# Optimization experiments

Measured on AMD Instinct MI355X. Metric: run time of the kernel, lower is better.

## Reference

```python
import jax, jax.numpy as jnp
import numpy as np
from jax import lax

K_ITERS = 35

def _conv3x3_same(x, w, b):
    # x: [B,1,H,W], w: [1,1,3,3]
    y = lax.conv_general_dilated(x, w, window_strides=(1, 1),
                                 padding=((1, 1), (1, 1)),
                                 dimension_numbers=('NCHW', 'OIHW', 'NCHW'))
    return y + b.reshape(1, -1, 1, 1)

def _maxpool3x3_same(v):
    # 3x3 max pool, stride 1, padding 1 (torch MaxPool2d(kernel=3, stride=1, padding=1))
    return lax.reduce_window(v, -jnp.inf, lax.max,
                             window_dimensions=(1, 1, 3, 3),
                             window_strides=(1, 1, 1, 1),
                             padding=((0, 0), (0, 0), (1, 1), (1, 1)))

def setup_inputs() -> dict:
    key = jax.random.key(0)
    k1, k2, k3 = jax.random.split(key, 3)
    B, H, W = 64, 192, 192
    X = jax.random.uniform(k1, (B, 2, H, W), dtype=jnp.float32)  # grid, goal in [0,1)
    hp_w = jax.random.uniform(k2, (1, 1, 3, 3), dtype=jnp.float32) * 0.5
    p_w = jax.random.uniform(k3, (1, 1, 3, 3), dtype=jnp.float32) * 0.5
    hp_b = jnp.zeros((1,), dtype=jnp.float32)
    p_b = jnp.zeros((1,), dtype=jnp.float32)
    return {"X": X, "hp_w": hp_w, "hp_b": hp_b, "p_w": p_w, "p_b": p_b}

def reference(X, hp_w, hp_b, p_w, p_b):
    grid = X[:, 0:1]           # [B,1,H,W]
    goal = X[:, 1:2]           # [B,1,H,W]
    r = -(1.0 - goal)          # reward map in [-1, 0]
    # process_image: double conv -> wall/flow probability p in (0,1)
    h = jax.nn.relu(_conv3x3_same(grid, hp_w, hp_b))
    p = jax.nn.sigmoid(_conv3x3_same(h, p_w, p_b))
    # value iteration: v = max(v, r + p * (maxpool(v) - r)), k=35 steps
    def body(_, v):
        return jnp.maximum(v, r + p * (_maxpool3x3_same(v) - r))
    v = lax.fori_loop(0, K_ITERS, body, r)
    return (v[:, 0], p[:, 0])  # squeeze channel dim -> ([B,H,W], [B,H,W])
```

## Files before the change

### kernel.cpp

```cpp
#include <hip/hip_runtime.h>

#define HH 192
#define WW 192
#define HW 36864
#define BB 64
#define NPIX 2359296
#define NCH 48
#define NEG (-1.0e30f)

__device__ __forceinline__ float4 conv3x3_chunk(const float* __restrict__ img,
                                                int y, int ch, const float* __restrict__ w9,
                                                float bias) {
  float4 acc = make_float4(bias, bias, bias, bias);
  int x0 = ch * 4;
#pragma unroll
  for (int dy = -1; dy <= 1; ++dy) {
    int yy = y + dy;
    if (yy < 0 || yy >= HH) continue;
    const float* row = img + yy * WW + x0;
    float4 v = *reinterpret_cast<const float4*>(row);
    float l = (ch > 0) ? row[-1] : 0.f;
    float r = (ch < NCH - 1) ? row[4] : 0.f;
    float wa = w9[(dy + 1) * 3 + 0];
    float wb = w9[(dy + 1) * 3 + 1];
    float wc = w9[(dy + 1) * 3 + 2];
    acc.x += wa * l   + wb * v.x + wc * v.y;
    acc.y += wa * v.x + wb * v.y + wc * v.z;
    acc.z += wa * v.y + wb * v.z + wc * v.w;
    acc.w += wa * v.z + wb * v.w + wc * r;
  }
  return acc;
}

__global__ __launch_bounds__(256) void k_conv_h(const float* __restrict__ X,
                                                const float* __restrict__ w9,
                                                const float* __restrict__ b1,
                                                float* __restrict__ h) {
  int idx = blockIdx.x * 256 + threadIdx.x;
  if (idx >= NPIX / 4) return;
  int b = idx / (HW / 4);
  int rem = idx - b * (HW / 4);
  int y = rem / NCH;
  int ch = rem - y * NCH;
  float4 acc = conv3x3_chunk(X + (size_t)b * (2 * HW), y, ch, w9, b1[0]);
  acc.x = fmaxf(acc.x, 0.f); acc.y = fmaxf(acc.y, 0.f);
  acc.z = fmaxf(acc.z, 0.f); acc.w = fmaxf(acc.w, 0.f);
  *reinterpret_cast<float4*>(h + (size_t)b * HW + y * WW + ch * 4) = acc;
}

__global__ __launch_bounds__(256) void k_conv_p(const float* __restrict__ h,
                                                const float* __restrict__ w9,
                                                const float* __restrict__ b1,
                                                float* __restrict__ p_out) {
  int idx = blockIdx.x * 256 + threadIdx.x;
  if (idx >= NPIX / 4) return;
  int b = idx / (HW / 4);
  int rem = idx - b * (HW / 4);
  int y = rem / NCH;
  int ch = rem - y * NCH;
  float4 acc = conv3x3_chunk(h + (size_t)b * HW, y, ch, w9, b1[0]);
  acc.x = 1.f / (1.f + __expf(-acc.x));
  acc.y = 1.f / (1.f + __expf(-acc.y));
  acc.z = 1.f / (1.f + __expf(-acc.z));
  acc.w = 1.f / (1.f + __expf(-acc.w));
  *reinterpret_cast<float4*>(p_out + (size_t)b * HW + y * WW + ch * 4) = acc;
}

template <int FIRST>
__global__ __launch_bounds__(256, 1) void k_span(const float* __restrict__ v_in,
                                                 const float* __restrict__ p_glob,
                                                 const float* __restrict__ X,
                                                 float* __restrict__ v_out) {
  int wid = blockIdx.x * 4 + (threadIdx.x >> 6);
  int lane = threadIdx.x & 63;
  int b = wid >> 4;
  int t = wid & 15;
  int ti = t >> 2, tj = t & 3;
  int ly = lane >> 3, lx = lane & 7;
  int py = ti * 48 - 8 + ly * 8;
  int px = tj * 48 - 8 + lx * 8;
  bool colok = (px >= 0 && px < WW);

  const float* gimg = X + (size_t)b * (2 * HW) + HW;
  const float* pimg = p_glob + (size_t)b * HW;
  const float* vimg = v_in + (size_t)b * HW;

  float v[8][8], p[8][8], c[8][8];
#pragma unroll
  for (int r = 0; r < 8; ++r) {
    int gy = py + r;
    if (colok && gy >= 0 && gy < HH) {
      float4 g0 = *(const float4*)(gimg + gy * WW + px);
      float4 g1 = *(const float4*)(gimg + gy * WW + px + 4);
      float4 p0 = *(const float4*)(pimg + gy * WW + px);
      float4 p1 = *(const float4*)(pimg + gy * WW + px + 4);
      float gg[8] = {g0.x, g0.y, g0.z, g0.w, g1.x, g1.y, g1.z, g1.w};
      float pp[8] = {p0.x, p0.y, p0.z, p0.w, p1.x, p1.y, p1.z, p1.w};
#pragma unroll
      for (int j = 0; j < 8; ++j) {
        p[r][j] = pp[j];
        c[r][j] = (gg[j] - 1.f) * (1.f - pp[j]);
      }
      if (FIRST) {
#pragma unroll
        for (int j = 0; j < 8; ++j) v[r][j] = gg[j] - 1.f;
      } else {
        float4 v0 = *(const float4*)(vimg + gy * WW + px);
        float4 v1 = *(const float4*)(vimg + gy * WW + px + 4);
        v[r][0] = v0.x; v[r][1] = v0.y; v[r][2] = v0.z; v[r][3] = v0.w;
        v[r][4] = v1.x; v[r][5] = v1.y; v[r][6] = v1.z; v[r][7] = v1.w;
      }
    } else {
#pragma unroll
      for (int j = 0; j < 8; ++j) { v[r][j] = NEG; p[r][j] = 0.f; c[r][j] = NEG; }
    }
  }

  int lup = (lane - 8) & 63, ldn = (lane + 8) & 63;
  int llt = (lane - 1) & 63, lrt = (lane + 1) & 63;

#pragma unroll 1
  for (int it = 0; it < 7; ++it) {
    float th[8], bh[8];
#pragma unroll
    for (int j = 0; j < 8; ++j) { float s = __shfl(v[7][j], lup, 64); th[j] = (ly == 0) ? NEG : s; }
#pragma unroll
    for (int j = 0; j < 8; ++j) { float s = __shfl(v[0][j], ldn, 64); bh[j] = (ly == 7) ? NEG : s; }
    float vm[8][8];
#pragma unroll
    for (int r = 0; r < 8; ++r) {
#pragma unroll
      for (int j = 0; j < 8; ++j) {
        float up = (r == 0) ? th[j] : v[r - 1][j];
        float dn = (r == 7) ? bh[j] : v[r + 1][j];
        vm[r][j] = fmaxf(fmaxf(up, dn), v[r][j]);
      }
    }
#pragma unroll
    for (int r = 0; r < 8; ++r) {
      float sl = __shfl(vm[r][7], llt, 64);
      float sr = __shfl(vm[r][0], lrt, 64);
      float lvm = (lx == 0) ? NEG : sl;
      float rvm = (lx == 7) ? NEG : sr;
      float hm0 = fmaxf(lvm, fmaxf(vm[r][0], vm[r][1]));
      float hm7 = fmaxf(vm[r][6], fmaxf(vm[r][7], rvm));
      v[r][0] = fmaxf(v[r][0], fmaf(p[r][0], hm0, c[r][0]));
#pragma unroll
      for (int j = 1; j < 7; ++j) {
        float hm = fmaxf(vm[r][j - 1], fmaxf(vm[r][j], vm[r][j + 1]));
        v[r][j] = fmaxf(v[r][j], fmaf(p[r][j], hm, c[r][j]));
      }
      v[r][7] = fmaxf(v[r][7], fmaf(p[r][7], hm7, c[r][7]));
    }
  }

  if (ly >= 1 && ly <= 6 && lx >= 1 && lx <= 6) {
    float* wimg = v_out + (size_t)b * HW;
#pragma unroll
    for (int r = 0; r < 8; ++r) {
      *(float4*)(wimg + (py + r) * WW + px) = make_float4(v[r][0], v[r][1], v[r][2], v[r][3]);
      *(float4*)(wimg + (py + r) * WW + px + 4) = make_float4(v[r][4], v[r][5], v[r][6], v[r][7]);
    }
  }
}

extern "C" void kernel_launch(void* const* d_in, const int* in_sizes, int n_in,
                              void* d_out, int out_size, void* d_ws, size_t ws_size,
                              hipStream_t stream) {
  const float* X = (const float*)d_in[0];
  const float* hp_w = (const float*)d_in[1];
  const float* hp_b = (const float*)d_in[2];
  const float* p_w = (const float*)d_in[3];
  const float* p_b = (const float*)d_in[4];

  float* out = (float*)d_out;
  float* out_v = out;
  float* out_p = out + NPIX;
  float* bufA = (float*)d_ws;

  float* h = out_v;

  int nblk = (NPIX / 4 + 255) / 256;
  k_conv_h<<<nblk, 256, 0, stream>>>(X, hp_w, hp_b, h);
  k_conv_p<<<nblk, 256, 0, stream>>>(h, p_w, p_b, out_p);

  k_span<1><<<256, 256, 0, stream>>>(X , out_p, X, out_v);
  k_span<0><<<256, 256, 0, stream>>>(out_v, out_p, X, bufA);
  k_span<0><<<256, 256, 0, stream>>>(bufA, out_p, X, out_v);
  k_span<0><<<256, 256, 0, stream>>>(out_v, out_p, X, bufA);
  k_span<0><<<256, 256, 0, stream>>>(bufA, out_p, X, out_v);
}
```

Measured before the change: 166.4 us.

## Fuse the two 3x3 convolutions into one kernel and batch span loads

Replaces the separate relu-conv and sigmoid-conv kernels with one fused kernel that loads a 5-row window of the grid and recomputes the intermediate h tile in registers. This removes the h write and re-read through global memory and one kernel launch, at the cost of redundant h computation per thread. The span kernel's initial loads are also reordered so all p, goal and v loads are issued before the arithmetic, to increase memory-level parallelism.

```diff
diff --git a/kernel.cpp b/kernel.cpp
--- a/kernel.cpp
+++ b/kernel.cpp
@@ -5,65 +5,74 @@
 #define HW 36864
 #define BB 64
 #define NPIX 2359296
-#define NCH 48
 #define NEG (-1.0e30f)
 
-__device__ __forceinline__ float4 conv3x3_chunk(const float* __restrict__ img,
-                                                int y, int ch, const float* __restrict__ w9,
-                                                float bias) {
-  float4 acc = make_float4(bias, bias, bias, bias);
-  int x0 = ch * 4;
-#pragma unroll
-  for (int dy = -1; dy <= 1; ++dy) {
-    int yy = y + dy;
-    if (yy < 0 || yy >= HH) continue;
-    const float* row = img + yy * WW + x0;
-    float4 v = *reinterpret_cast<const float4*>(row);
-    float l = (ch > 0) ? row[-1] : 0.f;
-    float r = (ch < NCH - 1) ? row[4] : 0.f;
-    float wa = w9[(dy + 1) * 3 + 0];
-    float wb = w9[(dy + 1) * 3 + 1];
-    float wc = w9[(dy + 1) * 3 + 2];
-    acc.x += wa * l   + wb * v.x + wc * v.y;
-    acc.y += wa * v.x + wb * v.y + wc * v.z;
-    acc.z += wa * v.y + wb * v.z + wc * v.w;
-    acc.w += wa * v.z + wb * v.w + wc * r;
-  }
-  return acc;
-}
-
-__global__ __launch_bounds__(256) void k_conv_h(const float* __restrict__ X,
-                                                const float* __restrict__ w9,
-                                                const float* __restrict__ b1,
-                                                float* __restrict__ h) {
+__global__ __launch_bounds__(256) void k_conv_fused(const float* __restrict__ X,
+                                                    const float* __restrict__ hw9,
+                                                    const float* __restrict__ hb,
+                                                    const float* __restrict__ pw9,
+                                                    const float* __restrict__ pb,
+                                                    float* __restrict__ p_out) {
   int idx = blockIdx.x * 256 + threadIdx.x;
   if (idx >= NPIX / 4) return;
   int b = idx / (HW / 4);
   int rem = idx - b * (HW / 4);
-  int y = rem / NCH;
-  int ch = rem - y * NCH;
-  float4 acc = conv3x3_chunk(X + (size_t)b * (2 * HW), y, ch, w9, b1[0]);
-  acc.x = fmaxf(acc.x, 0.f); acc.y = fmaxf(acc.y, 0.f);
-  acc.z = fmaxf(acc.z, 0.f); acc.w = fmaxf(acc.w, 0.f);
-  *reinterpret_cast<float4*>(h + (size_t)b * HW + y * WW + ch * 4) = acc;
-}
-
-__global__ __launch_bounds__(256) void k_conv_p(const float* __restrict__ h,
-                                                const float* __restrict__ w9,
-                                                const float* __restrict__ b1,
-                                                float* __restrict__ p_out) {
-  int idx = blockIdx.x * 256 + threadIdx.x;
-  if (idx >= NPIX / 4) return;
-  int b = idx / (HW / 4);
-  int rem = idx - b * (HW / 4);
-  int y = rem / NCH;
-  int ch = rem - y * NCH;
-  float4 acc = conv3x3_chunk(h + (size_t)b * HW, y, ch, w9, b1[0]);
-  acc.x = 1.f / (1.f + __expf(-acc.x));
-  acc.y = 1.f / (1.f + __expf(-acc.y));
-  acc.z = 1.f / (1.f + __expf(-acc.z));
-  acc.w = 1.f / (1.f + __expf(-acc.w));
-  *reinterpret_cast<float4*>(p_out + (size_t)b * HW + y * WW + ch * 4) = acc;
+  int y = rem / 48;
+  int ch = rem - y * 48;
+  int x0 = ch * 4;
+  const float* g = X + (size_t)b * (2 * HW);
+
+  float gr[5][8];
+#pragma unroll
+  for (int ry = 0; ry < 5; ++ry) {
+    int yy = y - 2 + ry;
+    if (yy < 0 || yy >= HH) {
+#pragma unroll
+      for (int j = 0; j < 8; ++j) gr[ry][j] = 0.f;
+    } else {
+      const float* row = g + yy * WW;
+      float4 a = (x0 >= 4) ? *(const float4*)(row + x0 - 4) : make_float4(0, 0, 0, 0);
+      float4 m = *(const float4*)(row + x0);
+      float4 cq = (x0 + 4 < WW) ? *(const float4*)(row + x0 + 4) : make_float4(0, 0, 0, 0);
+      gr[ry][0] = a.z; gr[ry][1] = a.w;
+      gr[ry][2] = m.x; gr[ry][3] = m.y; gr[ry][4] = m.z; gr[ry][5] = m.w;
+      gr[ry][6] = cq.x; gr[ry][7] = cq.y;
+    }
+  }
+  float hwv[9], pwv[9];
+#pragma unroll
+  for (int i = 0; i < 9; ++i) { hwv[i] = hw9[i]; pwv[i] = pw9[i]; }
+  float hbv = hb[0], pbv = pb[0];
+
+  float hr[3][6];
+#pragma unroll
+  for (int ry = 0; ry < 3; ++ry) {
+    int yy = y - 1 + ry;
+    bool rowok = (yy >= 0 && yy < HH);
+#pragma unroll
+    for (int j = 0; j < 6; ++j) {
+      int xx = x0 - 1 + j;
+      float acc = hbv;
+#pragma unroll
+      for (int di = 0; di < 3; ++di)
+#pragma unroll
+        for (int dj = 0; dj < 3; ++dj)
+          acc = fmaf(gr[ry + di][j + dj], hwv[di * 3 + dj], acc);
+      hr[ry][j] = (rowok && xx >= 0 && xx < WW) ? fmaxf(acc, 0.f) : 0.f;
+    }
+  }
+  float o[4];
+#pragma unroll
+  for (int k = 0; k < 4; ++k) {
+    float acc = pbv;
+#pragma unroll
+    for (int di = 0; di < 3; ++di)
+#pragma unroll
+      for (int dj = 0; dj < 3; ++dj)
+        acc = fmaf(hr[di][k + dj], pwv[di * 3 + dj], acc);
+    o[k] = 1.f / (1.f + __expf(-acc));
+  }
+  *(float4*)(p_out + (size_t)b * HW + y * WW + x0) = make_float4(o[0], o[1], o[2], o[3]);
 }
 
 template <int FIRST>
@@ -86,29 +95,43 @@
   const float* vimg = v_in + (size_t)b * HW;
 
   float v[8][8], p[8][8], c[8][8];
+
 #pragma unroll
   for (int r = 0; r < 8; ++r) {
     int gy = py + r;
     if (colok && gy >= 0 && gy < HH) {
-      float4 g0 = *(const float4*)(gimg + gy * WW + px);
-      float4 g1 = *(const float4*)(gimg + gy * WW + px + 4);
-      float4 p0 = *(const float4*)(pimg + gy * WW + px);
-      float4 p1 = *(const float4*)(pimg + gy * WW + px + 4);
-      float gg[8] = {g0.x, g0.y, g0.z, g0.w, g1.x, g1.y, g1.z, g1.w};
-      float pp[8] = {p0.x, p0.y, p0.z, p0.w, p1.x, p1.y, p1.z, p1.w};
+      *(float4*)&p[r][0] = *(const float4*)(pimg + gy * WW + px);
+      *(float4*)&p[r][4] = *(const float4*)(pimg + gy * WW + px + 4);
+    }
+  }
+#pragma unroll
+  for (int r = 0; r < 8; ++r) {
+    int gy = py + r;
+    if (colok && gy >= 0 && gy < HH) {
+      *(float4*)&c[r][0] = *(const float4*)(gimg + gy * WW + px);
+      *(float4*)&c[r][4] = *(const float4*)(gimg + gy * WW + px + 4);
+    }
+  }
+  if (!FIRST) {
+#pragma unroll
+    for (int r = 0; r < 8; ++r) {
+      int gy = py + r;
+      if (colok && gy >= 0 && gy < HH) {
+        *(float4*)&v[r][0] = *(const float4*)(vimg + gy * WW + px);
+        *(float4*)&v[r][4] = *(const float4*)(vimg + gy * WW + px + 4);
+      }
+    }
+  }
+
+#pragma unroll
+  for (int r = 0; r < 8; ++r) {
+    int gy = py + r;
+    if (colok && gy >= 0 && gy < HH) {
 #pragma unroll
       for (int j = 0; j < 8; ++j) {
-        p[r][j] = pp[j];
-        c[r][j] = (gg[j] - 1.f) * (1.f - pp[j]);
-      }
-      if (FIRST) {
-#pragma unroll
-        for (int j = 0; j < 8; ++j) v[r][j] = gg[j] - 1.f;
-      } else {
-        float4 v0 = *(const float4*)(vimg + gy * WW + px);
-        float4 v1 = *(const float4*)(vimg + gy * WW + px + 4);
-        v[r][0] = v0.x; v[r][1] = v0.y; v[r][2] = v0.z; v[r][3] = v0.w;
-        v[r][4] = v1.x; v[r][5] = v1.y; v[r][6] = v1.z; v[r][7] = v1.w;
+        float gg = c[r][j];
+        if (FIRST) v[r][j] = gg - 1.f;
+        c[r][j] = (gg - 1.f) * (1.f - p[r][j]);
       }
     } else {
 #pragma unroll
@@ -178,11 +201,8 @@
   float* out_p = out + NPIX;
   float* bufA = (float*)d_ws;
 
-  float* h = out_v;
-
   int nblk = (NPIX / 4 + 255) / 256;
-  k_conv_h<<<nblk, 256, 0, stream>>>(X, hp_w, hp_b, h);
-  k_conv_p<<<nblk, 256, 0, stream>>>(h, p_w, p_b, out_p);
+  k_conv_fused<<<nblk, 256, 0, stream>>>(X, hp_w, hp_b, p_w, p_b, out_p);
 
   k_span<1><<<256, 256, 0, stream>>>(X , out_p, X, out_v);
   k_span<0><<<256, 256, 0, stream>>>(out_v, out_p, X, bufA);
```

Result: faster. 160.8 us (-3.3%).
